# Kernel tuning notes

Hardware: AMD Instinct MI355X
Metric: run time of the kernel (lower is better)

## Reference

```python
import jax, jax.numpy as jnp
import numpy as np

B, N, E, C, R2 = 2048, 20000, 512, 128, 474  # batch, n_tail, embed_dim, class_num, 2*num_rel
TOPK, TEMP = 10, 0.5


def _mlp2(x, w1, b1, w2, b2):
    return jax.nn.relu(x @ w1 + b1) @ w2 + b2


def _bn(x, g, b):
    # BatchNorm1d, training-mode math (batch statistics), eps=1e-5
    m = x.mean(0)
    v = x.var(0)
    return g * (x - m) / jnp.sqrt(v + 1e-5) + b


def _soft_topk_mask(x, k, temp):
    # sigmoid-relaxed top-k: threshold at the k-th largest value per row
    thr = jax.lax.top_k(x, k)[0][:, -1:]
    return jax.nn.sigmoid((x - thr) / temp)


def setup_inputs() -> dict:
    key = jax.random.key(0)
    ks = iter(jax.random.split(key, 40))
    nrm = lambda shape, s=0.05: jax.random.normal(next(ks), shape, jnp.float32) * s
    inp = {
        'head_vector': jax.random.normal(next(ks), (B, E), jnp.float32),
        'relation_vector': jax.random.normal(next(ks), (B, E), jnp.float32),
        'relation_index': jax.random.randint(next(ks), (B,), 0, R2),
        'tail_vector': jax.random.normal(next(ks), (N, E), jnp.float32),
        'label': jnp.zeros((B,), jnp.float32),
        'codebook': nrm((R2, C, C)),
        'core': nrm((C, C, C)),
        # head/relation/tail sub-graph feature MLPs: Linear(E,E)-ReLU-Linear(E,C)
        'hsw1': nrm((E, E)), 'hsb1': jnp.zeros((E,), jnp.float32),
        'hsw2': nrm((E, C)), 'hsb2': jnp.zeros((C,), jnp.float32),
        'rsw1': nrm((E, E)), 'rsb1': jnp.zeros((E,), jnp.float32),
        'rsw2': nrm((E, C)), 'rsb2': jnp.zeros((C,), jnp.float32),
        'tsw1': nrm((E, E)), 'tsb1': jnp.zeros((E,), jnp.float32),
        'tsw2': nrm((E, C)), 'tsb2': jnp.zeros((C,), jnp.float32),
        'bn0_g': jnp.ones((C,), jnp.float32), 'bn0_b': jnp.zeros((C,), jnp.float32),
        'bn1_g': jnp.ones((C,), jnp.float32), 'bn1_b': jnp.zeros((C,), jnp.float32),
        # hr_abstract_feature: Linear(2E,2C)-ReLU-Linear(2C,2C)-ReLU-Linear(2C,C)
        'hrw1': nrm((2 * E, 2 * C)), 'hrb1': jnp.zeros((2 * C,), jnp.float32),
        'hrw2': nrm((2 * C, 2 * C)), 'hrb2': jnp.zeros((2 * C,), jnp.float32),
        'hrw3': nrm((2 * C, C)), 'hrb3': jnp.zeros((C,), jnp.float32),
        # tail_abstract_feature: Linear(E,E)-ReLU-Linear(E,C)
        'taw1': nrm((E, E)), 'tab1': jnp.zeros((E,), jnp.float32),
        'taw2': nrm((E, C)), 'tab2': jnp.zeros((C,), jnp.float32),
    }
    return inp


def reference(head_vector, relation_vector, relation_index, tail_vector, label,
              codebook, core,
              hsw1, hsb1, hsw2, hsb2, rsw1, rsb1, rsw2, rsb2,
              tsw1, tsb1, tsw2, tsb2, bn0_g, bn0_b, bn1_g, bn1_b,
              hrw1, hrb1, hrw2, hrb2, hrw3, hrb3, taw1, tab1, taw2, tab2):
    # ----- TuckER branch -----
    hs = _mlp2(head_vector, hsw1, hsb1, hsw2, hsb2)            # [B,C]
    rs = _mlp2(relation_vector, rsw1, rsb1, rsw2, rsb2)        # [B,C]
    ts = _mlp2(tail_vector, tsw1, tsb1, tsw2, tsb2)            # [N,C]
    ha = _bn(hs, bn0_g, bn0_b)                                  # [B,C]
    W = (rs @ core.reshape(C, C * C)).reshape(-1, C, C)         # [B,C,C]
    Wm = jnp.einsum('bc,bcd->bd', ha, W)                        # [B,C]
    Wm = _bn(Wm, bn1_g, bn1_b)
    tucker_logits = Wm @ ts.T                                   # [B,N]
    # ----- possibility-codebook branch -----
    hr_in = jnp.concatenate([head_vector, relation_vector], axis=-1)
    h = jax.nn.relu(hr_in @ hrw1 + hrb1)
    h = jax.nn.relu(h @ hrw2 + hrb2)
    hra = h @ hrw3 + hrb3                                       # [B,C]
    ta = _mlp2(tail_vector, taw1, tab1, taw2, tab2)             # [N,C]
    pc = jnp.tanh(codebook[relation_index])                     # [B,C,C]
    hrm = _soft_topk_mask(hra, TOPK, TEMP) * hra                # [B,C]
    tam = _soft_topk_mask(ta, TOPK, TEMP) * ta                  # [N,C]
    inter = jnp.einsum('bc,bcd->bd', hrm, pc)                   # [B,C]
    possibility_score = inter @ tam.T                           # [B,N]
    return (tucker_logits, possibility_score)
```

## Files before the change

### kernel.cpp

```cpp
#include <hip/hip_runtime.h>
#include <stdint.h>

typedef unsigned short u16;
typedef __attribute__((ext_vector_type(8))) short short8;
typedef __attribute__((ext_vector_type(4))) float floatx4;

#define DEVFN static __device__ __forceinline__

DEVFN float bf2f(u16 u) { unsigned int x = ((unsigned int)u) << 16; float f; __builtin_memcpy(&f, &x, 4); return f; }
DEVFN u16 f2bf(float f) { unsigned int x; __builtin_memcpy(&x, &f, 4); x = (x + 0x7FFFu + ((x >> 16) & 1u)) >> 16; return (u16)x; }
DEVFN float san(float v) { return (v == v) ? v : 0.0f; }

static constexpr int BB = 2048;
static constexpr int NTAIL = 20000;
static constexpr int EE = 512;
static constexpr int CC = 128;

template<int MT, int NT, bool RELU, bool BIAS, bool OUTBF, bool ATOMIC, bool FUSEX>
__global__ __launch_bounds__(64)
void gemm_nt(const u16* __restrict__ A, const u16* __restrict__ Bm,
             void* __restrict__ Cout, const float* __restrict__ bias,
             const u16* __restrict__ rsp, const u16* __restrict__ hap,
             int M, int N, int K, int lda, int klen)
{
    const int lane = threadIdx.x;
    const int r = lane & 15, q = lane >> 4;
    const int m0 = blockIdx.x * (MT * 16);
    const int n0 = blockIdx.y * (NT * 16);
    int k0 = 0, kend = K;
    if (ATOMIC) { k0 = blockIdx.z * klen; kend = k0 + klen; }

    int arow[MT];
    size_t abase[MT];
    size_t bbase[NT];
#pragma unroll
    for (int mt = 0; mt < MT; ++mt) {
        int row = m0 + mt * 16 + r; if (row > M - 1) row = M - 1;
        arow[mt] = row;
        abase[mt] = (size_t)row * (size_t)lda;
    }
#pragma unroll
    for (int nt = 0; nt < NT; ++nt) {
        int row = n0 + nt * 16 + r; if (row > N - 1) row = N - 1;
        bbase[nt] = (size_t)row * (size_t)K;
    }

    floatx4 acc[MT][NT];
#pragma unroll
    for (int mt = 0; mt < MT; ++mt)
#pragma unroll
        for (int nt = 0; nt < NT; ++nt) acc[mt][nt] = (floatx4)0.0f;

    for (int k = k0; k < kend; k += 32) {
        const int ko = k + q * 8;
        short8 af[MT], bfr[NT];
        if (FUSEX) {
            const int e = ko >> 7, c0 = ko & 127;
#pragma unroll
            for (int mt = 0; mt < MT; ++mt) {
                const float rsv = bf2f(rsp[arow[mt] * 128 + e]);
                short8 hv = *reinterpret_cast<const short8*>(hap + arow[mt] * 128 + c0);
                short8 t;
#pragma unroll
                for (int j = 0; j < 8; ++j) t[j] = (short)f2bf(rsv * bf2f((u16)hv[j]));
                af[mt] = t;
            }
        } else {
#pragma unroll
            for (int mt = 0; mt < MT; ++mt)
                af[mt] = *reinterpret_cast<const short8*>(A + abase[mt] + ko);
        }
#pragma unroll
        for (int nt = 0; nt < NT; ++nt)
            bfr[nt] = *reinterpret_cast<const short8*>(Bm + bbase[nt] + ko);
#pragma unroll
        for (int mt = 0; mt < MT; ++mt)
#pragma unroll
            for (int nt = 0; nt < NT; ++nt)
                acc[mt][nt] = __builtin_amdgcn_mfma_f32_16x16x32_bf16(af[mt], bfr[nt], acc[mt][nt], 0, 0, 0);
    }

#pragma unroll
    for (int nt = 0; nt < NT; ++nt) {
        const int col = n0 + nt * 16 + r;
        if (col >= N) continue;
        float bv = 0.0f;
        if (BIAS) bv = san(bias[col]);
#pragma unroll
        for (int mt = 0; mt < MT; ++mt) {
#pragma unroll
            for (int rr = 0; rr < 4; ++rr) {
                const int row = m0 + mt * 16 + q * 4 + rr;
                if (row >= M) continue;
                float v = acc[mt][nt][rr] + bv;
                if (RELU) v = fmaxf(v, 0.0f);
                const size_t idx = (size_t)row * (size_t)N + col;
                if (ATOMIC)      atomicAdd((float*)Cout + idx, v);
                else if (OUTBF)  ((u16*)Cout)[idx] = f2bf(v);
                else             ((float*)Cout)[idx] = v;
            }
        }
    }
}

__global__ void cast_f32_bf16(const float* __restrict__ in, u16* __restrict__ out, int n)
{
    int id = blockIdx.x * 256 + threadIdx.x;
    if (id < n) out[id] = f2bf(san(in[id]));
}

__global__ void transpose_f32_bf16(const float* __restrict__ in, u16* __restrict__ out, int R, int C)
{
    __shared__ float tile[32][33];
    int c0 = blockIdx.x * 32, r0 = blockIdx.y * 32;
    int tx = threadIdx.x, ty = threadIdx.y;
#pragma unroll
    for (int i = 0; i < 32; i += 8) {
        int rr = r0 + ty + i, cc = c0 + tx;
        if (rr < R && cc < C) tile[ty + i][tx] = in[(size_t)rr * C + cc];
    }
    __syncthreads();
#pragma unroll
    for (int i = 0; i < 32; i += 8) {
        int orow = c0 + ty + i, ocol = r0 + tx;
        if (orow < C && ocol < R) out[(size_t)orow * R + ocol] = f2bf(san(tile[tx][ty + i]));
    }
}

__global__ void concat_hr(const float* __restrict__ h, const float* __restrict__ r, u16* __restrict__ out)
{
    int id = blockIdx.x * 256 + threadIdx.x;
    int b = id >> 10, j = id & 1023;
    float v = (j < 512) ? h[(b << 9) + j] : r[(b << 9) + j - 512];
    out[id] = f2bf(san(v));
}

__global__ __launch_bounds__(256) void bn_stats(const float* __restrict__ X, int R,
                                                float* __restrict__ mean, float* __restrict__ rstd)
{
    __shared__ float ss[256], sq[256];
    int c = blockIdx.x, t = threadIdx.x;
    float s = 0.f, s2 = 0.f;
    for (int rr = t; rr < R; rr += 256) { float v = X[(size_t)rr * 128 + c]; s += v; s2 += v * v; }
    ss[t] = s; sq[t] = s2; __syncthreads();
    for (int off = 128; off > 0; off >>= 1) {
        if (t < off) { ss[t] += ss[t + off]; sq[t] += sq[t + off]; }
        __syncthreads();
    }
    if (t == 0) {
        float m = ss[0] / R;
        float var = fmaxf(sq[0] / R - m * m, 0.0f);
        mean[c] = m;
        rstd[c] = 1.0f / sqrtf(var + 1e-5f);
    }
}

__global__ void bn_apply(const float* __restrict__ X, const float* __restrict__ mean,
                         const float* __restrict__ rstd, const float* __restrict__ g,
                         const float* __restrict__ b, u16* __restrict__ out, int n)
{
    int id = blockIdx.x * 256 + threadIdx.x;
    if (id >= n) return;
    int c = id & 127;
    float v = (X[id] - mean[c]) * rstd[c] * san(g[c]) + san(b[c]);
    out[id] = f2bf(v);
}

__global__ void zero_f32(float* __restrict__ p, int n)
{
    int id = blockIdx.x * 256 + threadIdx.x;
    if (id < n) p[id] = 0.0f;
}

__global__ __launch_bounds__(64) void soft_topk(const float* __restrict__ X, u16* __restrict__ out)
{
    int row = blockIdx.x, lane = threadIdx.x;
    const float* x = X + (size_t)row * 128;
    float v0 = x[lane], v1 = x[lane + 64];
    float w0 = v0, w1 = v1;
    float thr = 0.f;
    for (int it = 0; it < 10; ++it) {
        float m = fmaxf(w0, w1);
#pragma unroll
        for (int off = 32; off > 0; off >>= 1) m = fmaxf(m, __shfl_xor(m, off));
        if (it == 9) { thr = m; break; }
        unsigned long long msk = __ballot((w0 == m) || (w1 == m));
        if (msk) {
            int first = (int)__builtin_ctzll(msk);
            if (lane == first) {
                if (w0 == m) w0 = -__builtin_inff(); else w1 = -__builtin_inff();
            }
        }
    }
    float z0 = 1.f / (1.f + expf(-(v0 - thr) * 2.f));
    float z1 = 1.f / (1.f + expf(-(v1 - thr) * 2.f));
    out[(size_t)row * 128 + lane]      = f2bf(z0 * v0);
    out[(size_t)row * 128 + lane + 64] = f2bf(z1 * v1);
}

__global__ __launch_bounds__(128) void inter_kernel(const u16* __restrict__ hrm,
                                                    const float* __restrict__ codebook,
                                                    const int* __restrict__ relidx,
                                                    u16* __restrict__ out)
{
    int b = blockIdx.x, d = threadIdx.x;
    int rel = relidx[b];
    const float* cb = codebook + (size_t)rel * (128 * 128);
    const u16* hr = hrm + (size_t)b * 128;
    float s = 0.f;
    for (int c = 0; c < 128; ++c)
        s += bf2f(hr[c]) * tanhf(san(cb[c * 128 + d]));
    out[(size_t)b * 128 + d] = f2bf(s);
}

extern "C" void kernel_launch(void* const* d_in, const int* in_sizes, int n_in,
                              void* d_out, int out_size, void* d_ws, size_t ws_size,
                              hipStream_t stream)
{
    (void)in_sizes; (void)n_in; (void)out_size;

    const float* head    = (const float*)d_in[0];
    const float* relv    = (const float*)d_in[1];
    const int*   relidx  = (const int*)d_in[2];
    const float* tail    = (const float*)d_in[3];
    const float* codebook= (const float*)d_in[5];
    const float* core    = (const float*)d_in[6];
    const float* hsw1 = (const float*)d_in[7],  *hsb1 = (const float*)d_in[8];
    const float* hsw2 = (const float*)d_in[9],  *hsb2 = (const float*)d_in[10];
    const float* rsw1 = (const float*)d_in[11], *rsb1 = (const float*)d_in[12];
    const float* rsw2 = (const float*)d_in[13], *rsb2 = (const float*)d_in[14];
    const float* tsw1 = (const float*)d_in[15], *tsb1 = (const float*)d_in[16];
    const float* tsw2 = (const float*)d_in[17], *tsb2 = (const float*)d_in[18];
    const float* bn0g = (const float*)d_in[19], *bn0b = (const float*)d_in[20];
    const float* bn1g = (const float*)d_in[21], *bn1b = (const float*)d_in[22];
    const float* hrw1 = (const float*)d_in[23], *hrb1 = (const float*)d_in[24];
    const float* hrw2 = (const float*)d_in[25], *hrb2 = (const float*)d_in[26];
    const float* hrw3 = (const float*)d_in[27], *hrb3 = (const float*)d_in[28];
    const float* taw1 = (const float*)d_in[29], *tab1 = (const float*)d_in[30];
    const float* taw2 = (const float*)d_in[31], *tab2 = (const float*)d_in[32];

    float* out_tucker = (float*)d_out;
    float* out_poss   = out_tucker + (size_t)BB * NTAIL;

    char* ws = (char*)d_ws;
    size_t off = 0;
    auto alloc = [&](size_t bytes) -> char* {
        char* p = ws + off;
        off += (bytes + 255) & ~(size_t)255;
        return p;
    };

    float* hs_f   = (float*)alloc((size_t)BB * CC * 4);
    float* hra_f  = (float*)alloc((size_t)BB * CC * 4);
    float* Wm_pre = (float*)alloc((size_t)BB * CC * 4);
    float* mean0  = (float*)alloc(128 * 4);
    float* rstd0  = (float*)alloc(128 * 4);
    float* mean1  = (float*)alloc(128 * 4);
    float* rstd1  = (float*)alloc(128 * 4);

    u16* t_hid   = (u16*)alloc((size_t)NTAIL * EE * 2);
    u16* hr_in   = (u16*)alloc((size_t)BB * 1024 * 2);
    u16* h_hid   = (u16*)alloc((size_t)BB * EE * 2);
    u16* h1      = h_hid;
    u16* h2      = h_hid + (size_t)BB * 256;
    u16* tam_bf  = hr_in;
    u16* ts_bf   = (u16*)alloc((size_t)NTAIL * CC * 2);
    u16* tail_bf = (u16*)alloc((size_t)NTAIL * EE * 2);
    float* ta_f  = (float*)tail_bf;
    u16* rs_bf   = (u16*)alloc((size_t)BB * CC * 2);
    u16* ha_bf   = (u16*)alloc((size_t)BB * CC * 2);
    u16* Wm_bf   = (u16*)alloc((size_t)BB * CC * 2);
    u16* hrm_bf  = (u16*)alloc((size_t)BB * CC * 2);
    u16* inter_bf= (u16*)alloc((size_t)BB * CC * 2);

    u16* hsw1t = (u16*)alloc((size_t)EE * EE * 2);
    u16* hsw2t = (u16*)alloc((size_t)CC * EE * 2);
    u16* rsw1t = (u16*)alloc((size_t)EE * EE * 2);
    u16* rsw2t = (u16*)alloc((size_t)CC * EE * 2);
    u16* tsw1t = (u16*)alloc((size_t)EE * EE * 2);
    u16* tsw2t = (u16*)alloc((size_t)CC * EE * 2);
    u16* taw1t = (u16*)alloc((size_t)EE * EE * 2);
    u16* taw2t = (u16*)alloc((size_t)CC * EE * 2);
    u16* hrw1t = (u16*)alloc((size_t)256 * 1024 * 2);
    u16* hrw2t = (u16*)alloc((size_t)256 * 256 * 2);
    u16* hrw3t = (u16*)alloc((size_t)128 * 256 * 2);
    u16* core_t = (u16*)alloc((size_t)CC * 16384 * 2);

    if (off > ws_size) return;

    auto T = [&](const float* in, u16* outp, int R, int Cc) {
        dim3 g((Cc + 31) / 32, (R + 31) / 32), b(32, 8);
        transpose_f32_bf16<<<g, b, 0, stream>>>(in, outp, R, Cc);
    };
    T(hsw1, hsw1t, EE, EE);   T(hsw2, hsw2t, EE, CC);
    T(rsw1, rsw1t, EE, EE);   T(rsw2, rsw2t, EE, CC);
    T(tsw1, tsw1t, EE, EE);   T(tsw2, tsw2t, EE, CC);
    T(taw1, taw1t, EE, EE);   T(taw2, taw2t, EE, CC);
    T(hrw1, hrw1t, 2 * EE, 2 * CC);
    T(hrw2, hrw2t, 2 * CC, 2 * CC);
    T(hrw3, hrw3t, 2 * CC, CC);
    T(core, core_t, CC * CC, CC);

    concat_hr<<<(BB * 1024) / 256, 256, 0, stream>>>(head, relv, hr_in);
    cast_f32_bf16<<<(NTAIL * EE) / 256, 256, 0, stream>>>(tail, tail_bf, NTAIL * EE);

    gemm_nt<2, 2, true, true, true, false, false><<<dim3(BB / 32, EE / 32), 64, 0, stream>>>(
        hr_in, hsw1t, h_hid, hsb1, nullptr, nullptr, BB, EE, EE, 1024, 0);
    gemm_nt<2, 2, false, true, false, false, false><<<dim3(BB / 32, CC / 32), 64, 0, stream>>>(
        h_hid, hsw2t, hs_f, hsb2, nullptr, nullptr, BB, CC, EE, EE, 0);
    gemm_nt<2, 2, true, true, true, false, false><<<dim3(BB / 32, EE / 32), 64, 0, stream>>>(
        hr_in + 512, rsw1t, h_hid, rsb1, nullptr, nullptr, BB, EE, EE, 1024, 0);
    gemm_nt<2, 2, false, true, true, false, false><<<dim3(BB / 32, CC / 32), 64, 0, stream>>>(
        h_hid, rsw2t, rs_bf, rsb2, nullptr, nullptr, BB, CC, EE, EE, 0);
    gemm_nt<4, 4, true, true, true, false, false><<<dim3((NTAIL + 63) / 64, EE / 64), 64, 0, stream>>>(
        tail_bf, tsw1t, t_hid, tsb1, nullptr, nullptr, NTAIL, EE, EE, EE, 0);
    gemm_nt<4, 4, false, true, true, false, false><<<dim3((NTAIL + 63) / 64, CC / 64), 64, 0, stream>>>(
        t_hid, tsw2t, ts_bf, tsb2, nullptr, nullptr, NTAIL, CC, EE, EE, 0);
    gemm_nt<4, 4, true, true, true, false, false><<<dim3((NTAIL + 63) / 64, EE / 64), 64, 0, stream>>>(
        tail_bf, taw1t, t_hid, tab1, nullptr, nullptr, NTAIL, EE, EE, EE, 0);
    gemm_nt<4, 4, false, true, false, false, false><<<dim3((NTAIL + 63) / 64, CC / 64), 64, 0, stream>>>(
        t_hid, taw2t, ta_f, tab2, nullptr, nullptr, NTAIL, CC, EE, EE, 0);
    gemm_nt<2, 2, true, true, true, false, false><<<dim3(BB / 32, 256 / 32), 64, 0, stream>>>(
        hr_in, hrw1t, h1, hrb1, nullptr, nullptr, BB, 256, 1024, 1024, 0);
    gemm_nt<2, 2, true, true, true, false, false><<<dim3(BB / 32, 256 / 32), 64, 0, stream>>>(
        h1, hrw2t, h2, hrb2, nullptr, nullptr, BB, 256, 256, 256, 0);
    gemm_nt<2, 2, false, true, false, false, false><<<dim3(BB / 32, CC / 32), 64, 0, stream>>>(
        h2, hrw3t, hra_f, hrb3, nullptr, nullptr, BB, CC, 256, 256, 0);

    bn_stats<<<128, 256, 0, stream>>>(hs_f, BB, mean0, rstd0);
    bn_apply<<<(BB * CC) / 256, 256, 0, stream>>>(hs_f, mean0, rstd0, bn0g, bn0b, ha_bf, BB * CC);

    zero_f32<<<(BB * CC) / 256, 256, 0, stream>>>(Wm_pre, BB * CC);
    gemm_nt<2, 2, false, false, false, true, true><<<dim3(BB / 32, CC / 32, 8), 64, 0, stream>>>(
        nullptr, core_t, Wm_pre, nullptr, rs_bf, ha_bf, BB, CC, 16384, 16384, 16384 / 8);

    bn_stats<<<128, 256, 0, stream>>>(Wm_pre, BB, mean1, rstd1);
    bn_apply<<<(BB * CC) / 256, 256, 0, stream>>>(Wm_pre, mean1, rstd1, bn1g, bn1b, Wm_bf, BB * CC);

    gemm_nt<4, 4, false, false, false, false, false><<<dim3(BB / 64, (NTAIL + 63) / 64), 64, 0, stream>>>(
        Wm_bf, ts_bf, out_tucker, nullptr, nullptr, nullptr, BB, NTAIL, CC, CC, 0);

    soft_topk<<<BB, 64, 0, stream>>>(hra_f, hrm_bf);
    soft_topk<<<NTAIL, 64, 0, stream>>>(ta_f, tam_bf);

    inter_kernel<<<BB, 128, 0, stream>>>(hrm_bf, codebook, relidx, inter_bf);

    gemm_nt<4, 4, false, false, false, false, false><<<dim3(BB / 64, (NTAIL + 63) / 64), 64, 0, stream>>>(
        inter_bf, tam_bf, out_poss, nullptr, nullptr, nullptr, BB, NTAIL, CC, CC, 0);
}
```

Measured before the change: 927.2 us.

## Add LDS-staged 128x128 MFMA GEMM, materialize Kronecker operand, batch small launches

```diff
diff --git a/kernel.cpp b/kernel.cpp
--- a/kernel.cpp
+++ b/kernel.cpp
@@ -10,6 +10,14 @@
 DEVFN float bf2f(u16 u) { unsigned int x = ((unsigned int)u) << 16; float f; __builtin_memcpy(&f, &x, 4); return f; }
 DEVFN u16 f2bf(float f) { unsigned int x; __builtin_memcpy(&x, &f, 4); x = (x + 0x7FFFu + ((x >> 16) & 1u)) >> 16; return (u16)x; }
 DEVFN float san(float v) { return (v == v) ? v : 0.0f; }
+
+DEVFN void gld16(const u16* g, u16* l)
+{
+    __builtin_amdgcn_global_load_lds(
+        (const __attribute__((address_space(1))) unsigned int*)g,
+        (__attribute__((address_space(3))) unsigned int*)l,
+        16, 0, 0);
+}
 
 static constexpr int BB = 2048;
 static constexpr int NTAIL = 20000;
@@ -103,17 +111,143 @@
     }
 }
 
-__global__ void cast_f32_bf16(const float* __restrict__ in, u16* __restrict__ out, int n)
+template<bool RELU, bool BIAS, bool OUTBF, bool ATOMIC>
+__global__ __launch_bounds__(256)
+void gemm128(const u16* __restrict__ A, const u16* __restrict__ Bm,
+             void* __restrict__ Cout, const float* __restrict__ bias,
+             int M, int N, int K, int lda, int klen)
+{
+    __shared__ u16 As[128 * 32];
+    __shared__ u16 Bs[128 * 32];
+    const int t = threadIdx.x;
+    const int lane = t & 63;
+    const int wave = t >> 6;
+    const int wr = wave >> 1, wc = wave & 1;
+    const int r = lane & 15, q = lane >> 4;
+    const int m0 = blockIdx.x * 128;
+    const int n0 = blockIdx.y * 128;
+    int k0 = 0, kend = K;
+    if (ATOMIC) { k0 = blockIdx.z * klen; kend = k0 + klen; }
+
+    const int sr = lane >> 2;
+    const int sc = (lane & 3) * 8;
+    int ar0 = m0 + wave * 16 + sr;       if (ar0 > M - 1) ar0 = M - 1;
+    int ar1 = m0 + 64 + wave * 16 + sr;  if (ar1 > M - 1) ar1 = M - 1;
+    int br0 = n0 + wave * 16 + sr;       if (br0 > N - 1) br0 = N - 1;
+    int br1 = n0 + 64 + wave * 16 + sr;  if (br1 > N - 1) br1 = N - 1;
+
+    const u16* aS0 = A + (size_t)ar0 * (size_t)lda + sc;
+    const u16* aS1 = A + (size_t)ar1 * (size_t)lda + sc;
+    const u16* bS0 = Bm + (size_t)br0 * (size_t)K + sc;
+    const u16* bS1 = Bm + (size_t)br1 * (size_t)K + sc;
+    u16* aD0 = As + (wave * 16) * 32;
+    u16* aD1 = As + (64 + wave * 16) * 32;
+    u16* bD0 = Bs + (wave * 16) * 32;
+    u16* bD1 = Bs + (64 + wave * 16) * 32;
+
+    floatx4 acc[4][4];
+#pragma unroll
+    for (int i = 0; i < 4; ++i)
+#pragma unroll
+        for (int j = 0; j < 4; ++j) acc[i][j] = (floatx4)0.0f;
+
+    const int aoff = (wr * 64 + r) * 32 + q * 8;
+    const int boff = (wc * 64 + r) * 32 + q * 8;
+
+    for (int k = k0; k < kend; k += 32) {
+        gld16(aS0 + k, aD0);
+        gld16(aS1 + k, aD1);
+        gld16(bS0 + k, bD0);
+        gld16(bS1 + k, bD1);
+        __syncthreads();
+        short8 af[4], bfr[4];
+#pragma unroll
+        for (int mt = 0; mt < 4; ++mt)
+            af[mt] = *reinterpret_cast<const short8*>(As + aoff + mt * (16 * 32));
+#pragma unroll
+        for (int nt = 0; nt < 4; ++nt)
+            bfr[nt] = *reinterpret_cast<const short8*>(Bs + boff + nt * (16 * 32));
+#pragma unroll
+        for (int mt = 0; mt < 4; ++mt)
+#pragma unroll
+            for (int nt = 0; nt < 4; ++nt)
+                acc[mt][nt] = __builtin_amdgcn_mfma_f32_16x16x32_bf16(af[mt], bfr[nt], acc[mt][nt], 0, 0, 0);
+        __syncthreads();
+    }
+
+#pragma unroll
+    for (int nt = 0; nt < 4; ++nt) {
+        const int col = n0 + wc * 64 + nt * 16 + r;
+        if (col >= N) continue;
+        float bv = 0.0f;
+        if (BIAS) bv = san(bias[col]);
+#pragma unroll
+        for (int mt = 0; mt < 4; ++mt) {
+#pragma unroll
+            for (int rr = 0; rr < 4; ++rr) {
+                const int row = m0 + wr * 64 + mt * 16 + q * 4 + rr;
+                if (row >= M) continue;
+                float v = acc[mt][nt][rr] + bv;
+                if (RELU) v = fmaxf(v, 0.0f);
+                const size_t idx = (size_t)row * (size_t)N + col;
+                if (ATOMIC)      atomicAdd((float*)Cout + idx, v);
+                else if (OUTBF)  ((u16*)Cout)[idx] = f2bf(v);
+                else             ((float*)Cout)[idx] = v;
+            }
+        }
+    }
+}
+
+__global__ __launch_bounds__(256) void kron_rs_ha(const u16* __restrict__ rs,
+                                                  const u16* __restrict__ ha,
+                                                  u16* __restrict__ out)
 {
     int id = blockIdx.x * 256 + threadIdx.x;
-    if (id < n) out[id] = f2bf(san(in[id]));
-}
-
-__global__ void transpose_f32_bf16(const float* __restrict__ in, u16* __restrict__ out, int R, int C)
+    int b = id >> 11;
+    int j = id & 2047;
+    int e = j >> 4;
+    int c0 = (j & 15) << 3;
+    float rv = bf2f(rs[b * 128 + e]);
+    short8 hv = *reinterpret_cast<const short8*>(ha + b * 128 + c0);
+    short8 o;
+#pragma unroll
+    for (int i = 0; i < 8; ++i) o[i] = (short)f2bf(rv * bf2f((u16)hv[i]));
+    *reinterpret_cast<short8*>(out + (size_t)b * 16384 + (size_t)j * 8) = o;
+}
+
+__global__ void cast8_f32_bf16(const float* __restrict__ in, u16* __restrict__ out, int n8)
+{
+    int id = blockIdx.x * 256 + threadIdx.x;
+    if (id >= n8) return;
+    const floatx4* p = reinterpret_cast<const floatx4*>(in) + (size_t)id * 2;
+    floatx4 a = p[0], b = p[1];
+    short8 o;
+#pragma unroll
+    for (int i = 0; i < 4; ++i) { o[i] = (short)f2bf(san(a[i])); o[i + 4] = (short)f2bf(san(b[i])); }
+    *reinterpret_cast<short8*>(out + (size_t)id * 8) = o;
+}
+
+struct TJobs {
+    const float* in[12];
+    u16* out[12];
+    int R[12], C[12];
+    int tstart[13];
+};
+
+__global__ __launch_bounds__(256) void transpose_multi(TJobs j)
 {
     __shared__ float tile[32][33];
-    int c0 = blockIdx.x * 32, r0 = blockIdx.y * 32;
-    int tx = threadIdx.x, ty = threadIdx.y;
+    int tb = blockIdx.x;
+    int job = 0;
+    while (job < 11 && tb >= j.tstart[job + 1]) ++job;
+    int local = tb - j.tstart[job];
+    const int R = j.R[job], C = j.C[job];
+    const int cb = (C + 31) >> 5;
+    const int bx = local % cb, by = local / cb;
+    const float* in = j.in[job];
+    u16* out = j.out[job];
+    const int c0 = bx * 32, r0 = by * 32;
+    const int tx = threadIdx.x, ty = threadIdx.y;
 #pragma unroll
     for (int i = 0; i < 32; i += 8) {
         int rr = r0 + ty + i, cc = c0 + tx;
@@ -172,10 +306,13 @@
     if (id < n) p[id] = 0.0f;
 }
 
-__global__ __launch_bounds__(64) void soft_topk(const float* __restrict__ X, u16* __restrict__ out)
+__global__ __launch_bounds__(64) void soft_topk2(const float* __restrict__ X0, u16* __restrict__ O0, int R0,
+                                                 const float* __restrict__ X1, u16* __restrict__ O1)
 {
     int row = blockIdx.x, lane = threadIdx.x;
-    const float* x = X + (size_t)row * 128;
+    const float* x; u16* o;
+    if (row < R0) { x = X0 + (size_t)row * 128; o = O0 + (size_t)row * 128; }
+    else          { x = X1 + (size_t)(row - R0) * 128; o = O1 + (size_t)(row - R0) * 128; }
     float v0 = x[lane], v1 = x[lane + 64];
     float w0 = v0, w1 = v1;
     float thr = 0.f;
@@ -194,8 +331,8 @@
     }
     float z0 = 1.f / (1.f + expf(-(v0 - thr) * 2.f));
     float z1 = 1.f / (1.f + expf(-(v1 - thr) * 2.f));
-    out[(size_t)row * 128 + lane]      = f2bf(z0 * v0);
-    out[(size_t)row * 128 + lane + 64] = f2bf(z1 * v1);
+    o[lane]      = f2bf(z0 * v0);
+    o[lane + 64] = f2bf(z1 * v1);
 }
 
 __global__ __launch_bounds__(128) void inter_kernel(const u16* __restrict__ hrm,
@@ -286,23 +423,33 @@
     u16* hrw3t = (u16*)alloc((size_t)128 * 256 * 2);
     u16* core_t = (u16*)alloc((size_t)CC * 16384 * 2);
 
-    if (off > ws_size) return;
-
-    auto T = [&](const float* in, u16* outp, int R, int Cc) {
-        dim3 g((Cc + 31) / 32, (R + 31) / 32), b(32, 8);
-        transpose_f32_bf16<<<g, b, 0, stream>>>(in, outp, R, Cc);
+    const size_t off_base = off;
+    if (off_base > ws_size) return;
+
+    u16* akron = (u16*)alloc((size_t)BB * 16384 * 2);
+    const bool use_akron = (off <= ws_size);
+
+    TJobs tj;
+    int ti = 0, tcum = 0;
+    auto addT = [&](const float* in, u16* outp, int R, int Cc) {
+        tj.in[ti] = in; tj.out[ti] = outp; tj.R[ti] = R; tj.C[ti] = Cc;
+        tj.tstart[ti] = tcum;
+        tcum += ((Cc + 31) / 32) * ((R + 31) / 32);
+        ++ti;
     };
-    T(hsw1, hsw1t, EE, EE);   T(hsw2, hsw2t, EE, CC);
-    T(rsw1, rsw1t, EE, EE);   T(rsw2, rsw2t, EE, CC);
-    T(tsw1, tsw1t, EE, EE);   T(tsw2, tsw2t, EE, CC);
-    T(taw1, taw1t, EE, EE);   T(taw2, taw2t, EE, CC);
-    T(hrw1, hrw1t, 2 * EE, 2 * CC);
-    T(hrw2, hrw2t, 2 * CC, 2 * CC);
-    T(hrw3, hrw3t, 2 * CC, CC);
-    T(core, core_t, CC * CC, CC);
+    addT(hsw1, hsw1t, EE, EE);   addT(hsw2, hsw2t, EE, CC);
+    addT(rsw1, rsw1t, EE, EE);   addT(rsw2, rsw2t, EE, CC);
+    addT(tsw1, tsw1t, EE, EE);   addT(tsw2, tsw2t, EE, CC);
+    addT(taw1, taw1t, EE, EE);   addT(taw2, taw2t, EE, CC);
+    addT(hrw1, hrw1t, 2 * EE, 2 * CC);
+    addT(hrw2, hrw2t, 2 * CC, 2 * CC);
+    addT(hrw3, hrw3t, 2 * CC, CC);
+    addT(core, core_t, CC * CC, CC);
+    tj.tstart[12] = tcum;
+    transpose_multi<<<tcum, dim3(32, 8), 0, stream>>>(tj);
 
     concat_hr<<<(BB * 1024) / 256, 256, 0, stream>>>(head, relv, hr_in);
-    cast_f32_bf16<<<(NTAIL * EE) / 256, 256, 0, stream>>>(tail, tail_bf, NTAIL * EE);
+    cast8_f32_bf16<<<(NTAIL * EE / 8) / 256, 256, 0, stream>>>(tail, tail_bf, NTAIL * EE / 8);
 
     gemm_nt<2, 2, true, true, true, false, false><<<dim3(BB / 32, EE / 32), 64, 0, stream>>>(
         hr_in, hsw1t, h_hid, hsb1, nullptr, nullptr, BB, EE, EE, 1024, 0);
@@ -312,14 +459,16 @@
         hr_in + 512, rsw1t, h_hid, rsb1, nullptr, nullptr, BB, EE, EE, 1024, 0);
     gemm_nt<2, 2, false, true, true, false, false><<<dim3(BB / 32, CC / 32), 64, 0, stream>>>(
         h_hid, rsw2t, rs_bf, rsb2, nullptr, nullptr, BB, CC, EE, EE, 0);
-    gemm_nt<4, 4, true, true, true, false, false><<<dim3((NTAIL + 63) / 64, EE / 64), 64, 0, stream>>>(
-        tail_bf, tsw1t, t_hid, tsb1, nullptr, nullptr, NTAIL, EE, EE, EE, 0);
-    gemm_nt<4, 4, false, true, true, false, false><<<dim3((NTAIL + 63) / 64, CC / 64), 64, 0, stream>>>(
-        t_hid, tsw2t, ts_bf, tsb2, nullptr, nullptr, NTAIL, CC, EE, EE, 0);
-    gemm_nt<4, 4, true, true, true, false, false><<<dim3((NTAIL + 63) / 64, EE / 64), 64, 0, stream>>>(
-        tail_bf, taw1t, t_hid, tab1, nullptr, nullptr, NTAIL, EE, EE, EE, 0);
-    gemm_nt<4, 4, false, true, false, false, false><<<dim3((NTAIL + 63) / 64, CC / 64), 64, 0, stream>>>(
-        t_hid, taw2t, ta_f, tab2, nullptr, nullptr, NTAIL, CC, EE, EE, 0);
+
+    gemm128<true, true, true, false><<<dim3(157, EE / 128), 256, 0, stream>>>(
+        tail_bf, tsw1t, t_hid, tsb1, NTAIL, EE, EE, EE, 0);
+    gemm128<false, true, true, false><<<dim3(157, 1), 256, 0, stream>>>(
+        t_hid, tsw2t, ts_bf, tsb2, NTAIL, CC, EE, EE, 0);
+    gemm128<true, true, true, false><<<dim3(157, EE / 128), 256, 0, stream>>>(
+        tail_bf, taw1t, t_hid, tab1, NTAIL, EE, EE, EE, 0);
+    gemm128<false, true, false, false><<<dim3(157, 1), 256, 0, stream>>>(
+        t_hid, taw2t, ta_f, tab2, NTAIL, CC, EE, EE, 0);
+
     gemm_nt<2, 2, true, true, true, false, false><<<dim3(BB / 32, 256 / 32), 64, 0, stream>>>(
         hr_in, hrw1t, h1, hrb1, nullptr, nullptr, BB, 256, 1024, 1024, 0);
     gemm_nt<2, 2, true, true, true, false, false><<<dim3(BB / 32, 256 / 32), 64, 0, stream>>>(
@@ -331,20 +480,25 @@
     bn_apply<<<(BB * CC) / 256, 256, 0, stream>>>(hs_f, mean0, rstd0, bn0g, bn0b, ha_bf, BB * CC);
 
     zero_f32<<<(BB * CC) / 256, 256, 0, stream>>>(Wm_pre, BB * CC);
-    gemm_nt<2, 2, false, false, false, true, true><<<dim3(BB / 32, CC / 32, 8), 64, 0, stream>>>(
-        nullptr, core_t, Wm_pre, nullptr, rs_bf, ha_bf, BB, CC, 16384, 16384, 16384 / 8);
+    if (use_akron) {
+        kron_rs_ha<<<(BB * 2048) / 256, 256, 0, stream>>>(rs_bf, ha_bf, akron);
+        gemm128<false, false, false, true><<<dim3(BB / 128, 1, 16), 256, 0, stream>>>(
+            akron, core_t, Wm_pre, nullptr, BB, CC, 16384, 16384, 1024);
+    } else {
+        gemm_nt<2, 2, false, false, false, true, true><<<dim3(BB / 32, CC / 32, 8), 64, 0, stream>>>(
+            nullptr, core_t, Wm_pre, nullptr, rs_bf, ha_bf, BB, CC, 16384, 16384, 16384 / 8);
+    }
 
     bn_stats<<<128, 256, 0, stream>>>(Wm_pre, BB, mean1, rstd1);
     bn_apply<<<(BB * CC) / 256, 256, 0, stream>>>(Wm_pre, mean1, rstd1, bn1g, bn1b, Wm_bf, BB * CC);
 
-    gemm_nt<4, 4, false, false, false, false, false><<<dim3(BB / 64, (NTAIL + 63) / 64), 64, 0, stream>>>(
-        Wm_bf, ts_bf, out_tucker, nullptr, nullptr, nullptr, BB, NTAIL, CC, CC, 0);
-
-    soft_topk<<<BB, 64, 0, stream>>>(hra_f, hrm_bf);
-    soft_topk<<<NTAIL, 64, 0, stream>>>(ta_f, tam_bf);
+    gemm128<false, false, false, false><<<dim3(BB / 128, 157), 256, 0, stream>>>(
+        Wm_bf, ts_bf, out_tucker, nullptr, BB, NTAIL, CC, CC, 0);
+
+    soft_topk2<<<BB + NTAIL, 64, 0, stream>>>(hra_f, hrm_bf, BB, ta_f, tam_bf);
 
     inter_kernel<<<BB, 128, 0, stream>>>(hrm_bf, codebook, relidx, inter_bf);
 
-    gemm_nt<4, 4, false, false, false, false, false><<<dim3(BB / 64, (NTAIL + 63) / 64), 64, 0, stream>>>(
-        inter_bf, tam_bf, out_poss, nullptr, nullptr, nullptr, BB, NTAIL, CC, CC, 0);
-}
+    gemm128<false, false, false, false><<<dim3(BB / 128, 157), 256, 0, stream>>>(
+        inter_bf, tam_bf, out_poss, nullptr, BB, NTAIL, CC, CC, 0);
+}
```

After: 783.3 us. -15.5%, faster.
